# Kernel tuning notes

Measured on AMD Instinct MI355X. Metric: run time of the kernel, lower is better.

The kernel has to match this reference:

```python
import jax, jax.numpy as jnp
import numpy as np

B, W, H = 16384, 16, 16
NUM_CLASSES = 1024
EMBED = 4
OUT = 1024

def setup_inputs() -> dict:
    key = jax.random.key(0)
    k0, k1, k2 = jax.random.split(key, 3)
    x = jax.random.randint(k0, (B, W, H), 0, NUM_CLASSES, dtype=jnp.int32)
    W_embed = jax.random.normal(k1, (NUM_CLASSES, EMBED), dtype=jnp.float32) * 0.02
    b_embed = jnp.zeros((EMBED,), dtype=jnp.float32)
    W_dense = jax.random.normal(k2, (EMBED * W * H, OUT), dtype=jnp.float32) * 0.02
    b_dense = jnp.zeros((OUT,), dtype=jnp.float32)
    return {"x": x, "W_embed": W_embed, "b_embed": b_embed, "W_dense": W_dense, "b_dense": b_dense}

def reference(x, W_embed, b_embed, W_dense, b_dense):
    # one_hot(x, C) @ W_embed + b_embed is mathematically a row-gather of W_embed
    emb = W_embed[x] + b_embed                 # (B, W, H, EMBED)
    flat = emb.reshape(emb.shape[0], -1)        # (B, W*H*EMBED)  == rearrange '... w h c -> ... (w h c)'
    return flat @ W_dense + b_dense             # (B, OUT)
```

## Files before the change

### kernel.cpp

```cpp
#include <hip/hip_runtime.h>
#include <stdint.h>
#include <stddef.h>

typedef __attribute__((ext_vector_type(8))) short bf16x8;
typedef __attribute__((ext_vector_type(4))) short bf16x4;
typedef __attribute__((ext_vector_type(4))) float f32x4;

typedef const __attribute__((address_space(1))) void* gptr1_t;
typedef __attribute__((address_space(3))) void* lptr3_t;

#define GLOAD_LDS16(gp, lp) \
  __builtin_amdgcn_global_load_lds((gptr1_t)(gp), (lptr3_t)(lp), 16, 0, 0)

__device__ __forceinline__ uint16_t f2bf(float f) {
  uint32_t u = __builtin_bit_cast(uint32_t, f);
  u += 0x7fffu + ((u >> 16) & 1u);
  return (uint16_t)(u >> 16);
}

#define MB   16384
#define NP   256
#define KDIM 1024
#define NDIM 1024
#define NCLS 1024

#define BM  128
#define BN  128
#define BK  64
#define NK  (KDIM / BK)


__global__ void build_bt_kernel(const float* __restrict__ Wd,
                                uint16_t* __restrict__ Btf) {
  __shared__ uint16_t tile[32][33];
  const int k0 = blockIdx.y * 32;
  const int n0 = blockIdx.x * 32;
  const int tx = threadIdx.x;
  const int ty = threadIdx.y;
  #pragma unroll
  for (int r = 0; r < 32; r += 8)
    tile[ty + r][tx] = f2bf(Wd[(size_t)(k0 + ty + r) * NDIM + n0 + tx]);
  __syncthreads();
  #pragma unroll
  for (int r = 0; r < 32; r += 8) {
    const int n = n0 + ty + r;
    const int k = k0 + tx;
    const int bn = n >> 7, g = (n >> 4) & 7, m = n & 15;
    const int kt = k >> 6, h = (k >> 5) & 1, q = (k >> 3) & 3, e = k & 7;
    Btf[(size_t)((bn * 16 + kt) * 2 + h) * 4096 + (size_t)(g * 64 + q * 16 + m) * 8 + e]
        = tile[tx][ty + r];
  }
}

__global__ __launch_bounds__(256) void fused_gemm_kernel(
    const int* __restrict__ x,
    const float* __restrict__ We,
    const float* __restrict__ be,
    const uint16_t* __restrict__ Btf,
    const float* __restrict__ bias,
    float* __restrict__ C) {
  __shared__ __align__(16) uint16_t web[NCLS * 4];
  __shared__ __align__(16) uint16_t As[2][4096];
  __shared__ __align__(16) uint16_t Bs[2][4096];

  const int tid  = threadIdx.x;
  const int bm   = blockIdx.x;
  const int bn   = blockIdx.y;
  const int wave = tid >> 6;
  const int lane = tid & 63;
  const int wr   = wave >> 1;
  const int wc   = wave & 1;
  const int lm   = lane & 15;
  const int q    = lane >> 4;

  const int row0 = bm * BM;
  const int col0 = bn * BN;

  {
    const float4 bb = *(const float4*)be;
    #pragma unroll
    for (int c0 = 0; c0 < NCLS; c0 += 256) {
      const int c = c0 + tid;
      const float4 w = *(const float4*)(We + (size_t)c * 4);
      bf16x4 t;
      t[0] = (short)f2bf(w.x + bb.x);
      t[1] = (short)f2bf(w.y + bb.y);
      t[2] = (short)f2bf(w.z + bb.z);
      t[3] = (short)f2bf(w.w + bb.w);
      *(bf16x4*)(web + (size_t)c * 4) = t;
    }
  }

  const int arow = tid >> 2;
  const int apos = (tid & 3) * 4;
  const int ah   = (tid >> 1) & 1;
  const int aq0  = (tid & 1) * 2;
  const int ag   = arow >> 4;
  const int am   = arow & 15;
  uint16_t* const da = As[ah] + (size_t)((ag    ) * 64 + aq0 * 16 + am) * 8;
  uint16_t* const db = As[ah] + (size_t)((ag + 4) * 64 + aq0 * 16 + am) * 8;

  f32x4 acc[4][4];
  #pragma unroll
  for (int i = 0; i < 4; i++)
    #pragma unroll
    for (int j = 0; j < 4; j++)
      acc[i][j] = (f32x4){0.f, 0.f, 0.f, 0.f};

  const int* xr_a = x + (size_t)(row0      + arow) * NP + apos;
  const int* xr_b = x + (size_t)(row0 + 64 + arow) * NP + apos;

  int4 xqa = *(const int4*)xr_a;
  int4 xqb = *(const int4*)xr_b;

  const uint16_t* const btb = Btf + (size_t)bn * (NK * 2 * 4096);

  __syncthreads();

  for (int kt = 0; kt < NK; ++kt) {
    const uint16_t* bsrc = btb + (size_t)kt * 2 * 4096;
    #pragma unroll
    for (int h = 0; h < 2; ++h) {
      GLOAD_LDS16(bsrc + (size_t)h * 4096 +        tid * 8, Bs[h] + tid * 8);
      GLOAD_LDS16(bsrc + (size_t)h * 4096 + 2048 + tid * 8, Bs[h] + 2048 + tid * 8);
    }

    {
      union { bf16x8 v; struct { bf16x4 lo, hi; } s; } u;
      u.s.lo = *(const bf16x4*)(web + ((unsigned)xqa.x * 4u));
      u.s.hi = *(const bf16x4*)(web + ((unsigned)xqa.y * 4u));
      *(bf16x8*)(da) = u.v;
      u.s.lo = *(const bf16x4*)(web + ((unsigned)xqa.z * 4u));
      u.s.hi = *(const bf16x4*)(web + ((unsigned)xqa.w * 4u));
      *(bf16x8*)(da + 128) = u.v;
      u.s.lo = *(const bf16x4*)(web + ((unsigned)xqb.x * 4u));
      u.s.hi = *(const bf16x4*)(web + ((unsigned)xqb.y * 4u));
      *(bf16x8*)(db) = u.v;
      u.s.lo = *(const bf16x4*)(web + ((unsigned)xqb.z * 4u));
      u.s.hi = *(const bf16x4*)(web + ((unsigned)xqb.w * 4u));
      *(bf16x8*)(db + 128) = u.v;
    }

    __syncthreads();

    if (kt + 1 < NK) {
      xqa = *(const int4*)(xr_a + (kt + 1) * 16);
      xqb = *(const int4*)(xr_b + (kt + 1) * 16);
    }

    #pragma unroll
    for (int h = 0; h < 2; ++h) {
      bf16x8 af[4], bfr[4];
      #pragma unroll
      for (int i = 0; i < 4; i++)
        af[i] = *(const bf16x8*)(As[h] + (size_t)((wr * 4 + i) * 64 + lane) * 8);
      #pragma unroll
      for (int j = 0; j < 4; j++)
        bfr[j] = *(const bf16x8*)(Bs[h] + (size_t)((wc * 4 + j) * 64 + lane) * 8);

      #pragma unroll
      for (int i = 0; i < 4; i++)
        #pragma unroll
        for (int j = 0; j < 4; j++)
          acc[i][j] = __builtin_amdgcn_mfma_f32_16x16x32_bf16(af[i], bfr[j], acc[i][j], 0, 0, 0);
    }

    __syncthreads();
  }

  float bvals[4];
  #pragma unroll
  for (int j = 0; j < 4; j++)
    bvals[j] = bias[col0 + wc * 64 + j * 16 + lm];

  #pragma unroll
  for (int i = 0; i < 4; i++) {
    const int rbase = row0 + wr * 64 + i * 16 + q * 4;
    #pragma unroll
    for (int j = 0; j < 4; j++) {
      const int col = col0 + wc * 64 + j * 16 + lm;
      #pragma unroll
      for (int r = 0; r < 4; r++)
        C[(size_t)(rbase + r) * NDIM + col] = acc[i][j][r] + bvals[j];
    }
  }
}

__global__ void naive_kernel(const int* __restrict__ x,
                             const float* __restrict__ We,
                             const float* __restrict__ be,
                             const float* __restrict__ Wd,
                             const float* __restrict__ bd,
                             float* __restrict__ out) {
  __shared__ float emb[KDIM];
  const int b = blockIdx.x;
  const int tid = threadIdx.x;
  {
    const int cls = x[(size_t)b * NP + tid];
    const float4 e  = *(const float4*)(We + (size_t)cls * 4);
    const float4 bb = *(const float4*)be;
    emb[tid * 4 + 0] = e.x + bb.x;
    emb[tid * 4 + 1] = e.y + bb.y;
    emb[tid * 4 + 2] = e.z + bb.z;
    emb[tid * 4 + 3] = e.w + bb.w;
  }
  __syncthreads();
  float acc0 = bd[tid], acc1 = bd[tid + 256], acc2 = bd[tid + 512], acc3 = bd[tid + 768];
  for (int k = 0; k < KDIM; ++k) {
    const float a = emb[k];
    const float* w = Wd + (size_t)k * NDIM + tid;
    acc0 += a * w[0];
    acc1 += a * w[256];
    acc2 += a * w[512];
    acc3 += a * w[768];
  }
  float* o = out + (size_t)b * NDIM + tid;
  o[0] = acc0; o[256] = acc1; o[512] = acc2; o[768] = acc3;
}

extern "C" void kernel_launch(void* const* d_in, const int* in_sizes, int n_in,
                              void* d_out, int out_size, void* d_ws, size_t ws_size,
                              hipStream_t stream) {
  const int*   x  = (const int*)d_in[0];
  const float* We = (const float*)d_in[1];
  const float* be = (const float*)d_in[2];
  const float* Wd = (const float*)d_in[3];
  const float* bd = (const float*)d_in[4];
  float* out = (float*)d_out;

  const size_t needB = (size_t)NDIM * KDIM * sizeof(uint16_t);

  if (ws_size >= needB) {
    uint16_t* Btw = (uint16_t*)d_ws;
    build_bt_kernel<<<dim3(NDIM / 32, KDIM / 32), dim3(32, 8), 0, stream>>>(Wd, Btw);
    fused_gemm_kernel<<<dim3(MB / BM, NDIM / BN), 256, 0, stream>>>(x, We, be, Btw, bd, out);
  } else {
    naive_kernel<<<MB, 256, 0, stream>>>(x, We, be, Wd, bd, out);
  }
}
```

Baseline: 134.0 us.

## Widen GEMM block tile to 128x256 with 8 waves per block

Doubles the N-dimension of the block tile to 256 and runs 512 threads (8 waves in a 2x4 grid), with the pre-packed B layout changed to match. Each block now reuses its gathered embedding A-tile across twice as many output columns, halving the redundant x-index loads and embedding gathers across the grid. The A-fill mapping is reworked so each thread gathers two 8-element fragments. The cost is more LDS per block and fewer blocks, which may lower occupancy.

```diff
diff --git a/kernel.cpp b/kernel.cpp
--- a/kernel.cpp
+++ b/kernel.cpp
@@ -25,7 +25,7 @@
 #define NCLS 1024
 
 #define BM  128
-#define BN  128
+#define BN  256
 #define BK  64
 #define NK  (KDIM / BK)
 
@@ -45,14 +45,14 @@
   for (int r = 0; r < 32; r += 8) {
     const int n = n0 + ty + r;
     const int k = k0 + tx;
-    const int bn = n >> 7, g = (n >> 4) & 7, m = n & 15;
+    const int bn = n >> 8, g = (n >> 4) & 15, m = n & 15;
     const int kt = k >> 6, h = (k >> 5) & 1, q = (k >> 3) & 3, e = k & 7;
-    Btf[(size_t)((bn * 16 + kt) * 2 + h) * 4096 + (size_t)(g * 64 + q * 16 + m) * 8 + e]
+    Btf[(size_t)((bn * 16 + kt) * 2 + h) * 8192 + (size_t)(g * 64 + q * 16 + m) * 8 + e]
         = tile[tx][ty + r];
   }
 }
 
-__global__ __launch_bounds__(256) void fused_gemm_kernel(
+__global__ __launch_bounds__(512) void fused_gemm_kernel(
     const int* __restrict__ x,
     const float* __restrict__ We,
     const float* __restrict__ be,
@@ -60,18 +60,18 @@
     const float* __restrict__ bias,
     float* __restrict__ C) {
   __shared__ __align__(16) uint16_t web[NCLS * 4];
-  __shared__ __align__(16) uint16_t As[2][4096];
-  __shared__ __align__(16) uint16_t Bs[2][4096];
+  __shared__ __align__(16) uint16_t As[2 * 4096];
+  __shared__ __align__(16) uint16_t Bs[2 * 8192];
 
   const int tid  = threadIdx.x;
   const int bm   = blockIdx.x;
   const int bn   = blockIdx.y;
-  const int wave = tid >> 6;
-  const int lane = tid & 63;
-  const int wr   = wave >> 1;
-  const int wc   = wave & 1;
-  const int lm   = lane & 15;
-  const int q    = lane >> 4;
+  const int w    = tid >> 6;
+  const int l    = tid & 63;
+  const int wr   = w >> 2;
+  const int wc   = w & 3;
+  const int lm   = l & 15;
+  const int q4   = l >> 4;
 
   const int row0 = bm * BM;
   const int col0 = bn * BN;
@@ -79,26 +79,24 @@
   {
     const float4 bb = *(const float4*)be;
     #pragma unroll
-    for (int c0 = 0; c0 < NCLS; c0 += 256) {
+    for (int c0 = 0; c0 < NCLS; c0 += 512) {
       const int c = c0 + tid;
-      const float4 w = *(const float4*)(We + (size_t)c * 4);
+      const float4 wv = *(const float4*)(We + (size_t)c * 4);
       bf16x4 t;
-      t[0] = (short)f2bf(w.x + bb.x);
-      t[1] = (short)f2bf(w.y + bb.y);
-      t[2] = (short)f2bf(w.z + bb.z);
-      t[3] = (short)f2bf(w.w + bb.w);
+      t[0] = (short)f2bf(wv.x + bb.x);
+      t[1] = (short)f2bf(wv.y + bb.y);
+      t[2] = (short)f2bf(wv.z + bb.z);
+      t[3] = (short)f2bf(wv.w + bb.w);
       *(bf16x4*)(web + (size_t)c * 4) = t;
     }
   }
 
-  const int arow = tid >> 2;
-  const int apos = (tid & 3) * 4;
-  const int ah   = (tid >> 1) & 1;
-  const int aq0  = (tid & 1) * 2;
-  const int ag   = arow >> 4;
-  const int am   = arow & 15;
-  uint16_t* const da = As[ah] + (size_t)((ag    ) * 64 + aq0 * 16 + am) * 8;
-  uint16_t* const db = As[ah] + (size_t)((ag + 4) * 64 + aq0 * 16 + am) * 8;
+  const int mh = w >> 2;
+  const int gb = (w & 3) * 2;
+  uint16_t* const dA0 = As + (size_t)mh * 4096 + (size_t)((gb    ) * 64 + l) * 8;
+  uint16_t* const dA1 = As + (size_t)mh * 4096 + (size_t)((gb + 1) * 64 + l) * 8;
+  const int* xr0 = x + (size_t)(row0 + (gb    ) * 16 + lm) * NP + mh * 8 + q4 * 2;
+  const int* xr1 = x + (size_t)(row0 + (gb + 1) * 16 + lm) * NP + mh * 8 + q4 * 2;
 
   f32x4 acc[4][4];
   #pragma unroll
@@ -107,45 +105,34 @@
     for (int j = 0; j < 4; j++)
       acc[i][j] = (f32x4){0.f, 0.f, 0.f, 0.f};
 
-  const int* xr_a = x + (size_t)(row0      + arow) * NP + apos;
-  const int* xr_b = x + (size_t)(row0 + 64 + arow) * NP + apos;
-
-  int4 xqa = *(const int4*)xr_a;
-  int4 xqb = *(const int4*)xr_b;
-
-  const uint16_t* const btb = Btf + (size_t)bn * (NK * 2 * 4096);
+  int2 xq0 = *(const int2*)xr0;
+  int2 xq1 = *(const int2*)xr1;
+
+  const uint16_t* const btb = Btf + (size_t)bn * (NK * 16384);
 
   __syncthreads();
 
   for (int kt = 0; kt < NK; ++kt) {
-    const uint16_t* bsrc = btb + (size_t)kt * 2 * 4096;
-    #pragma unroll
-    for (int h = 0; h < 2; ++h) {
-      GLOAD_LDS16(bsrc + (size_t)h * 4096 +        tid * 8, Bs[h] + tid * 8);
-      GLOAD_LDS16(bsrc + (size_t)h * 4096 + 2048 + tid * 8, Bs[h] + 2048 + tid * 8);
-    }
+    const uint16_t* bsrc = btb + (size_t)kt * 16384;
+    #pragma unroll
+    for (int r = 0; r < 4; ++r)
+      GLOAD_LDS16(bsrc + (size_t)r * 4096 + tid * 8, Bs + (size_t)r * 4096 + tid * 8);
 
     {
       union { bf16x8 v; struct { bf16x4 lo, hi; } s; } u;
-      u.s.lo = *(const bf16x4*)(web + ((unsigned)xqa.x * 4u));
-      u.s.hi = *(const bf16x4*)(web + ((unsigned)xqa.y * 4u));
-      *(bf16x8*)(da) = u.v;
-      u.s.lo = *(const bf16x4*)(web + ((unsigned)xqa.z * 4u));
-      u.s.hi = *(const bf16x4*)(web + ((unsigned)xqa.w * 4u));
-      *(bf16x8*)(da + 128) = u.v;
-      u.s.lo = *(const bf16x4*)(web + ((unsigned)xqb.x * 4u));
-      u.s.hi = *(const bf16x4*)(web + ((unsigned)xqb.y * 4u));
-      *(bf16x8*)(db) = u.v;
-      u.s.lo = *(const bf16x4*)(web + ((unsigned)xqb.z * 4u));
-      u.s.hi = *(const bf16x4*)(web + ((unsigned)xqb.w * 4u));
-      *(bf16x8*)(db + 128) = u.v;
+      u.s.lo = *(const bf16x4*)(web + ((unsigned)xq0.x * 4u));
+      u.s.hi = *(const bf16x4*)(web + ((unsigned)xq0.y * 4u));
+      *(bf16x8*)(dA0) = u.v;
+      u.s.lo = *(const bf16x4*)(web + ((unsigned)xq1.x * 4u));
+      u.s.hi = *(const bf16x4*)(web + ((unsigned)xq1.y * 4u));
+      *(bf16x8*)(dA1) = u.v;
     }
 
     __syncthreads();
 
     if (kt + 1 < NK) {
-      xqa = *(const int4*)(xr_a + (kt + 1) * 16);
-      xqb = *(const int4*)(xr_b + (kt + 1) * 16);
+      xq0 = *(const int2*)(xr0 + (kt + 1) * 16);
+      xq1 = *(const int2*)(xr1 + (kt + 1) * 16);
     }
 
     #pragma unroll
@@ -153,10 +140,10 @@
       bf16x8 af[4], bfr[4];
       #pragma unroll
       for (int i = 0; i < 4; i++)
-        af[i] = *(const bf16x8*)(As[h] + (size_t)((wr * 4 + i) * 64 + lane) * 8);
+        af[i] = *(const bf16x8*)(As + (size_t)h * 4096 + (size_t)((wr * 4 + i) * 64 + l) * 8);
       #pragma unroll
       for (int j = 0; j < 4; j++)
-        bfr[j] = *(const bf16x8*)(Bs[h] + (size_t)((wc * 4 + j) * 64 + lane) * 8);
+        bfr[j] = *(const bf16x8*)(Bs + (size_t)h * 8192 + (size_t)((wc * 4 + j) * 64 + l) * 8);
 
       #pragma unroll
       for (int i = 0; i < 4; i++)
@@ -175,7 +162,7 @@
 
   #pragma unroll
   for (int i = 0; i < 4; i++) {
-    const int rbase = row0 + wr * 64 + i * 16 + q * 4;
+    const int rbase = row0 + wr * 64 + i * 16 + q4 * 4;
     #pragma unroll
     for (int j = 0; j < 4; j++) {
       const int col = col0 + wc * 64 + j * 16 + lm;
@@ -208,11 +195,11 @@
   float acc0 = bd[tid], acc1 = bd[tid + 256], acc2 = bd[tid + 512], acc3 = bd[tid + 768];
   for (int k = 0; k < KDIM; ++k) {
     const float a = emb[k];
-    const float* w = Wd + (size_t)k * NDIM + tid;
-    acc0 += a * w[0];
-    acc1 += a * w[256];
-    acc2 += a * w[512];
-    acc3 += a * w[768];
+    const float* wv = Wd + (size_t)k * NDIM + tid;
+    acc0 += a * wv[0];
+    acc1 += a * wv[256];
+    acc2 += a * wv[512];
+    acc3 += a * wv[768];
   }
   float* o = out + (size_t)b * NDIM + tid;
   o[0] = acc0; o[256] = acc1; o[512] = acc2; o[768] = acc3;
@@ -233,7 +220,7 @@
   if (ws_size >= needB) {
     uint16_t* Btw = (uint16_t*)d_ws;
     build_bt_kernel<<<dim3(NDIM / 32, KDIM / 32), dim3(32, 8), 0, stream>>>(Wd, Btw);
-    fused_gemm_kernel<<<dim3(MB / BM, NDIM / BN), 256, 0, stream>>>(x, We, be, Btw, bd, out);
+    fused_gemm_kernel<<<dim3(MB / BM, NDIM / BN), 512, 0, stream>>>(x, We, be, Btw, bd, out);
   } else {
     naive_kernel<<<MB, 256, 0, stream>>>(x, We, be, Wd, bd, out);
   }
```

Result: faster. 123.5 us (-7.8%).
